# Kernel tuning notes

Measured on AMD Instinct MI355X. Metric: run time of the kernel, lower is better.

## Reference

```python
import jax, jax.numpy as jnp
import numpy as np

EMBED = 512
HEADS = 8
HEAD_DIM = EMBED // HEADS
N, T = 512, 64


def setup_inputs() -> dict:
    key = jax.random.key(0)
    ks = jax.random.split(key, 11)
    s = 1.0 / np.sqrt(EMBED)
    inp = {
        'values': jax.random.normal(ks[0], (N, T, EMBED), jnp.float32),
        'keys':   jax.random.normal(ks[1], (N, T, EMBED), jnp.float32),
        'query':  jax.random.normal(ks[2], (N, T, EMBED), jnp.float32),
        'Wv': jax.random.uniform(ks[3], (EMBED, EMBED), jnp.float32, -s, s),
        'bv': jax.random.uniform(ks[4], (EMBED,), jnp.float32, -s, s),
        'Wk': jax.random.uniform(ks[5], (EMBED, EMBED), jnp.float32, -s, s),
        'bk': jax.random.uniform(ks[6], (EMBED,), jnp.float32, -s, s),
        'Wq': jax.random.uniform(ks[7], (EMBED, EMBED), jnp.float32, -s, s),
        'bq': jax.random.uniform(ks[8], (EMBED,), jnp.float32, -s, s),
        'Wo': jax.random.uniform(ks[9], (EMBED, EMBED), jnp.float32, -s, s),
        'bo': jax.random.uniform(ks[10], (EMBED,), jnp.float32, -s, s),
    }
    return inp


def reference(values, keys, query, Wv, bv, Wk, bk, Wq, bq, Wo, bo):
    n, t, c = query.shape
    v = (values @ Wv.T + bv).reshape(n, t, HEADS, HEAD_DIM)
    k = (keys   @ Wk.T + bk).reshape(n, t, HEADS, HEAD_DIM)
    q = (query  @ Wq.T + bq).reshape(n, t, HEADS, HEAD_DIM)
    # attention over the batch axis: energy[q,k,t,h]
    energy = jnp.einsum('qthd,kthd->qkth', q, k)
    attn = jax.nn.softmax(energy / jnp.sqrt(jnp.float32(EMBED)), axis=1)
    out = jnp.einsum('qkth,kthd->qthd', attn, v).reshape(n, t, HEADS * HEAD_DIM)
    return out @ Wo.T + bo
```

## Files before the change

kernel.cpp:

```cpp
#include <hip/hip_runtime.h>
#include <hip/hip_bf16.h>
#include <math.h>

#define NBATCH 512
#define TT 64
#define EMB 512
#define NHEADS 8
#define HDIM 64
#define MROWS (NBATCH * TT)
#define ROWSTRIDE (TT * EMB)
#define WSEG 262144

static constexpr float QSCALE = 0.0637587140f;

typedef __attribute__((ext_vector_type(8))) short short8v;
typedef __attribute__((ext_vector_type(4))) float f32x4;

__device__ __forceinline__ unsigned short f2bf(float x) {
    union { float f; unsigned int u; } v; v.f = x;
    unsigned int r = v.u + 0x7fff + ((v.u >> 16) & 1);
    return (unsigned short)(r >> 16);
}

__device__ __forceinline__ unsigned int cvtpk(float lo, float hi) {
    unsigned int r;
    asm("v_cvt_pk_bf16_f32 %0, %1, %2" : "=v"(r) : "v"(lo), "v"(hi));
    return r;
}

__device__ __forceinline__ void gl16(const void* g, void* l) {
    __builtin_amdgcn_global_load_lds(
        (const __attribute__((address_space(1))) unsigned int*)g,
        (__attribute__((address_space(3))) unsigned int*)l, 16, 0, 0);
}

__global__ __launch_bounds__(256) void cvt3(
    const float* __restrict__ a, const float* __restrict__ b, const float* __restrict__ c,
    unsigned short* __restrict__ oa, unsigned short* __restrict__ ob, unsigned short* __restrict__ oc)
{
    const size_t i = (size_t)blockIdx.x * 256 + threadIdx.x;
    float4 va = reinterpret_cast<const float4*>(a)[i];
    float4 vb = reinterpret_cast<const float4*>(b)[i];
    float4 vc = reinterpret_cast<const float4*>(c)[i];
    ushort4 ra, rb, rc;
    ra.x = f2bf(va.x); ra.y = f2bf(va.y); ra.z = f2bf(va.z); ra.w = f2bf(va.w);
    rb.x = f2bf(vb.x); rb.y = f2bf(vb.y); rb.z = f2bf(vb.z); rb.w = f2bf(vb.w);
    rc.x = f2bf(vc.x); rc.y = f2bf(vc.y); rc.z = f2bf(vc.z); rc.w = f2bf(vc.w);
    reinterpret_cast<ushort4*>(oa)[i] = ra;
    reinterpret_cast<ushort4*>(ob)[i] = rb;
    reinterpret_cast<ushort4*>(oc)[i] = rc;
}

__global__ __launch_bounds__(256) void cvtw(
    const float* __restrict__ w0, const float* __restrict__ w1,
    const float* __restrict__ w2, const float* __restrict__ w3,
    unsigned short* __restrict__ dst)
{
    const int seg = blockIdx.y;
    const float* src = (seg == 0) ? w0 : (seg == 1) ? w1 : (seg == 2) ? w2 : w3;
    const float sc = (seg == 0) ? QSCALE : 1.0f;
    const size_t i = (size_t)blockIdx.x * 256 + threadIdx.x;
    float4 v = reinterpret_cast<const float4*>(src)[i];
    ushort4 r;
    r.x = f2bf(v.x * sc); r.y = f2bf(v.y * sc); r.z = f2bf(v.z * sc); r.w = f2bf(v.w * sc);
    reinterpret_cast<ushort4*>(dst + (size_t)seg * WSEG)[i] = r;
}

__global__ __launch_bounds__(256) void gemm_proj3(
    const unsigned short* __restrict__ A0, const unsigned short* __restrict__ A1,
    const unsigned short* __restrict__ A2, const unsigned short* __restrict__ Wb,
    const float* __restrict__ b0, const float* __restrict__ b1, const float* __restrict__ b2,
    unsigned short* __restrict__ o0, unsigned short* __restrict__ o1, unsigned short* __restrict__ o2)
{
    __shared__ __align__(16) unsigned short As[128 * 32];
    __shared__ __align__(16) unsigned short Bs[128 * 32];
    const int z = blockIdx.z;
    const unsigned short* A = (z == 0) ? A0 : (z == 1) ? A1 : A2;
    const unsigned short* W = Wb + (size_t)z * WSEG;
    const float* bias = (z == 0) ? b0 : (z == 1) ? b1 : b2;
    const float bsc = (z == 0) ? QSCALE : 1.0f;
    unsigned short* Cout = (z == 0) ? o0 : (z == 1) ? o1 : o2;

    const int tid = threadIdx.x;
    const int wave = tid >> 6, lane = tid & 63;
    const int lg = lane >> 4, li = lane & 15;
    const int m0 = blockIdx.x * 128;
    const int n0 = blockIdx.y * 128;
    const int wr = (wave >> 1) * 64;
    const int wc = (wave & 1) * 64;

    f32x4 acc[4][4] = {};

    const unsigned short* ga = A + (size_t)(m0 + (tid >> 2)) * 512 + (tid & 3) * 8;
    const unsigned short* gb = W + (size_t)(n0 + (tid >> 2)) * 512 + (tid & 3) * 8;
    unsigned short* lA = &As[wave * 512];
    unsigned short* lB = &Bs[wave * 512];

    for (int k0 = 0; k0 < 512; k0 += 32) {
        __syncthreads();
        gl16(ga + k0, lA);
        gl16(ga + k0 + 64 * 512, lA + 2048);
        gl16(gb + k0, lB);
        gl16(gb + k0 + 64 * 512, lB + 2048);
        __syncthreads();

        short8v af[4], bfr[4];
#pragma unroll
        for (int i = 0; i < 4; i++) {
            af[i]  = *reinterpret_cast<const short8v*>(&As[(wr + i * 16 + li) * 32 + lg * 8]);
            bfr[i] = *reinterpret_cast<const short8v*>(&Bs[(wc + i * 16 + li) * 32 + lg * 8]);
        }
#pragma unroll
        for (int i = 0; i < 4; i++)
#pragma unroll
            for (int j = 0; j < 4; j++)
                acc[i][j] = __builtin_amdgcn_mfma_f32_16x16x32_bf16(af[i], bfr[j], acc[i][j], 0, 0, 0);
    }

#pragma unroll
    for (int j = 0; j < 4; j++) {
        const int col = n0 + wc + j * 16 + li;
        const float bb = bias[col] * bsc;
#pragma unroll
        for (int i = 0; i < 4; i++) {
            const int row0 = m0 + wr + i * 16 + lg * 4;
#pragma unroll
            for (int r = 0; r < 4; r++)
                Cout[(size_t)(row0 + r) * 512 + col] = f2bf(acc[i][j][r] + bb);
        }
    }
}

__global__ __launch_bounds__(256) void gemm_out(
    const unsigned short* __restrict__ A, const unsigned short* __restrict__ W,
    const float* __restrict__ bias, float* __restrict__ Cout)
{
    __shared__ __align__(16) unsigned short As[128 * 32];
    __shared__ __align__(16) unsigned short Bs[128 * 32];
    const int tid = threadIdx.x;
    const int wave = tid >> 6, lane = tid & 63;
    const int lg = lane >> 4, li = lane & 15;
    const int m0 = blockIdx.x * 128;
    const int n0 = blockIdx.y * 128;
    const int wr = (wave >> 1) * 64;
    const int wc = (wave & 1) * 64;

    f32x4 acc[4][4] = {};

    const unsigned short* ga = A + (size_t)(m0 + (tid >> 2)) * 512 + (tid & 3) * 8;
    const unsigned short* gb = W + (size_t)(n0 + (tid >> 2)) * 512 + (tid & 3) * 8;
    unsigned short* lA = &As[wave * 512];
    unsigned short* lB = &Bs[wave * 512];

    for (int k0 = 0; k0 < 512; k0 += 32) {
        __syncthreads();
        gl16(ga + k0, lA);
        gl16(ga + k0 + 64 * 512, lA + 2048);
        gl16(gb + k0, lB);
        gl16(gb + k0 + 64 * 512, lB + 2048);
        __syncthreads();

        short8v af[4], bfr[4];
#pragma unroll
        for (int i = 0; i < 4; i++) {
            af[i]  = *reinterpret_cast<const short8v*>(&As[(wr + i * 16 + li) * 32 + lg * 8]);
            bfr[i] = *reinterpret_cast<const short8v*>(&Bs[(wc + i * 16 + li) * 32 + lg * 8]);
        }
#pragma unroll
        for (int i = 0; i < 4; i++)
#pragma unroll
            for (int j = 0; j < 4; j++)
                acc[i][j] = __builtin_amdgcn_mfma_f32_16x16x32_bf16(af[i], bfr[j], acc[i][j], 0, 0, 0);
    }

#pragma unroll
    for (int j = 0; j < 4; j++) {
        const int col = n0 + wc + j * 16 + li;
        const float bb = bias[col];
#pragma unroll
        for (int i = 0; i < 4; i++) {
            const int row0 = m0 + wr + i * 16 + lg * 4;
#pragma unroll
            for (int r = 0; r < 4; r++)
                Cout[(size_t)(row0 + r) * 512 + col] = acc[i][j][r] + bb;
        }
    }
}

__global__ __launch_bounds__(256) void attn_bf16(
    const unsigned short* __restrict__ qp, const unsigned short* __restrict__ kp,
    const unsigned short* __restrict__ vp, unsigned short* __restrict__ ao)
{
    __shared__ __align__(16) unsigned short Qs[128 * 64];
    __shared__ __align__(16) unsigned short Ks[64 * 64];
    __shared__ __align__(16) unsigned short Vt[64][68];
    __shared__ __align__(16) unsigned short Pl[4][32][72];

    const int tid = threadIdx.x;
    const int wave = tid >> 6, lane = tid & 63;
    const int lg = lane >> 4, li = lane & 15;
    const int n0 = blockIdx.x * 128;
    const int th = blockIdx.y;
    const size_t base = (size_t)(th >> 3) * EMB + (size_t)(th & 7) * HDIM;

    {
        const unsigned short* gq = qp + (size_t)(n0 + (tid >> 3)) * ROWSTRIDE + base + (tid & 7) * 8;
        unsigned short* lq = &Qs[wave * 512];
#pragma unroll
        for (int i = 0; i < 4; i++)
            gl16(gq + (size_t)i * 32 * ROWSTRIDE, lq + i * 2048);
    }
    __syncthreads();
    short8v qf[2][2];
#pragma unroll
    for (int mf = 0; mf < 2; mf++)
#pragma unroll
        for (int kf = 0; kf < 2; kf++)
            qf[mf][kf] = *reinterpret_cast<const short8v*>(
                &Qs[(wave * 32 + mf * 16 + li) * 64 + kf * 32 + lg * 8]);

    const int vd0 = (tid & 15) * 4;
    const int vk0 = (tid >> 4) * 4;
    const unsigned short* gv = vp + base + vd0;
    uint2 vl[4];
#pragma unroll
    for (int i = 0; i < 4; i++)
        vl[i] = *reinterpret_cast<const uint2*>(gv + (size_t)(vk0 + i) * ROWSTRIDE);

    const short8v ones = (short8v)(short)0x3F80;
    f32x4 acc[2][4] = {};
    f32x4 acc_l[2] = {};

    for (int kv = 0; kv < 8; kv++) {
        const int k0 = kv * 64;
        __syncthreads();

        {
            unsigned short* lk = &Ks[wave * 512];
#pragma unroll
            for (int i = 0; i < 2; i++) {
                const int r = (tid >> 3) + i * 32;
                const int srcofs = (((tid & 7) * 8) ^ ((r & 7) * 8));
                gl16(kp + (size_t)(k0 + r) * ROWSTRIDE + base + srcofs, lk + i * 2048);
            }
        }
#pragma unroll
        for (int dd = 0; dd < 4; dd++) {
            const unsigned int sel = (dd & 1) ? 0x07060302u : 0x05040100u;
            const unsigned int a = (dd < 2) ? vl[0].x : vl[0].y;
            const unsigned int b = (dd < 2) ? vl[1].x : vl[1].y;
            const unsigned int c = (dd < 2) ? vl[2].x : vl[2].y;
            const unsigned int d = (dd < 2) ? vl[3].x : vl[3].y;
            uint2 o;
            o.x = __builtin_amdgcn_perm(b, a, sel);
            o.y = __builtin_amdgcn_perm(d, c, sel);
            *reinterpret_cast<uint2*>(&Vt[vd0 + dd][vk0]) = o;
        }
        __syncthreads();

        if (kv < 7) {
#pragma unroll
            for (int i = 0; i < 4; i++)
                vl[i] = *reinterpret_cast<const uint2*>(
                    gv + (size_t)(k0 + 64 + vk0 + i) * ROWSTRIDE);
        }

        f32x4 s[2][4] = {};
#pragma unroll
        for (int nf = 0; nf < 4; nf++) {
            const int key = nf * 16 + li;
#pragma unroll
            for (int kf = 0; kf < 2; kf++) {
                const short8v kfrag = *reinterpret_cast<const short8v*>(
                    &Ks[key * 64 + ((kf * 32 + lg * 8) ^ ((key & 7) * 8))]);
#pragma unroll
                for (int mf = 0; mf < 2; mf++)
                    s[mf][nf] = __builtin_amdgcn_mfma_f32_16x16x32_bf16(kfrag, qf[mf][kf], s[mf][nf], 0, 0, 0);
            }
        }

#pragma unroll
        for (int mf = 0; mf < 2; mf++)
#pragma unroll
            for (int nf = 0; nf < 4; nf++) {
                const float p0 = exp2f(s[mf][nf][0]);
                const float p1 = exp2f(s[mf][nf][1]);
                const float p2 = exp2f(s[mf][nf][2]);
                const float p3 = exp2f(s[mf][nf][3]);
                union { unsigned int u[2]; uint2 v; } pk2;
                pk2.u[0] = cvtpk(p0, p1);
                pk2.u[1] = cvtpk(p2, p3);
                *reinterpret_cast<uint2*>(&Pl[wave][mf * 16 + li][nf * 16 + lg * 4]) = pk2.v;
            }

        short8v pf[2][2];
#pragma unroll
        for (int mf = 0; mf < 2; mf++)
#pragma unroll
            for (int kf = 0; kf < 2; kf++)
                pf[mf][kf] = *reinterpret_cast<const short8v*>(
                    &Pl[wave][mf * 16 + li][kf * 32 + lg * 8]);
#pragma unroll
        for (int mf = 0; mf < 2; mf++)
#pragma unroll
            for (int kf = 0; kf < 2; kf++)
                acc_l[mf] = __builtin_amdgcn_mfma_f32_16x16x32_bf16(pf[mf][kf], ones, acc_l[mf], 0, 0, 0);

#pragma unroll
        for (int df = 0; df < 4; df++)
#pragma unroll
            for (int kf = 0; kf < 2; kf++) {
                const short8v vfr = *reinterpret_cast<const short8v*>(
                    &Vt[df * 16 + li][kf * 32 + lg * 8]);
#pragma unroll
                for (int mf = 0; mf < 2; mf++)
                    acc[mf][df] = __builtin_amdgcn_mfma_f32_16x16x32_bf16(pf[mf][kf], vfr, acc[mf][df], 0, 0, 0);
            }
    }

#pragma unroll
    for (int mf = 0; mf < 2; mf++) {
#pragma unroll
        for (int r = 0; r < 4; r++) {
            const float linv = 1.0f / acc_l[mf][r];
            const int qrow = n0 + wave * 32 + mf * 16 + lg * 4 + r;
#pragma unroll
            for (int df = 0; df < 4; df++)
                ao[(size_t)qrow * ROWSTRIDE + base + df * 16 + li] = f2bf(acc[mf][df][r] * linv);
        }
    }
}

extern "C" void kernel_launch(void* const* d_in, const int* in_sizes, int n_in,
                              void* d_out, int out_size, void* d_ws, size_t ws_size,
                              hipStream_t stream) {
    const float* values = (const float*)d_in[0];
    const float* keys   = (const float*)d_in[1];
    const float* query  = (const float*)d_in[2];
    const float* Wv = (const float*)d_in[3];
    const float* bv = (const float*)d_in[4];
    const float* Wk = (const float*)d_in[5];
    const float* bk = (const float*)d_in[6];
    const float* Wq = (const float*)d_in[7];
    const float* bq = (const float*)d_in[8];
    const float* Wo = (const float*)d_in[9];
    const float* bo = (const float*)d_in[10];
    float* out = (float*)d_out;

    unsigned short* ws16 = (unsigned short*)d_ws;
    const size_t PLANE = (size_t)MROWS * EMB;
    unsigned short* xq = ws16;
    unsigned short* xk = ws16 + PLANE;
    unsigned short* xv = ws16 + 2 * PLANE;
    unsigned short* qb = ws16 + 3 * PLANE;
    unsigned short* kb = ws16 + 4 * PLANE;
    unsigned short* vb = ws16 + 5 * PLANE;
    unsigned short* ab = ws16 + 6 * PLANE;
    unsigned short* wb = ws16 + 7 * PLANE;

    cvt3<<<PLANE / 4 / 256, 256, 0, stream>>>(query, keys, values, xq, xk, xv);
    cvtw<<<dim3(WSEG / 4 / 256, 4), 256, 0, stream>>>(Wq, Wk, Wv, Wo, wb);

    gemm_proj3<<<dim3(MROWS / 128, EMB / 128, 3), 256, 0, stream>>>(
        xq, xk, xv, wb, bq, bk, bv, qb, kb, vb);

    attn_bf16<<<dim3(4, TT * NHEADS), 256, 0, stream>>>(qb, kb, vb, ab);

    gemm_out<<<dim3(MROWS / 128, EMB / 128), 256, 0, stream>>>(
        ab, wb + 3 * WSEG, bo, out);
}
```

Before: 245.7 us.

## Fuse fp32-to-bf16 activation conversion into projection GEMM A-tile load

Removes the separate cvt3 kernel, which read three fp32 activation planes and wrote bf16 copies. The projection GEMM now loads fp32 A tiles straight into LDS with an XOR-swizzled layout and converts them to bf16 with v_cvt_pk_bf16_f32 when building MFMA fragments. This drops one kernel launch and a full bf16 write plus re-read of the activations. In exchange each of the four column blocks reloads fp32 A (twice the bytes), LDS use doubles and conversion work moves inside the GEMM inner loop.

```diff
diff --git a/kernel.cpp b/kernel.cpp
--- a/kernel.cpp
+++ b/kernel.cpp
@@ -32,23 +32,6 @@
     __builtin_amdgcn_global_load_lds(
         (const __attribute__((address_space(1))) unsigned int*)g,
         (__attribute__((address_space(3))) unsigned int*)l, 16, 0, 0);
-}
-
-__global__ __launch_bounds__(256) void cvt3(
-    const float* __restrict__ a, const float* __restrict__ b, const float* __restrict__ c,
-    unsigned short* __restrict__ oa, unsigned short* __restrict__ ob, unsigned short* __restrict__ oc)
-{
-    const size_t i = (size_t)blockIdx.x * 256 + threadIdx.x;
-    float4 va = reinterpret_cast<const float4*>(a)[i];
-    float4 vb = reinterpret_cast<const float4*>(b)[i];
-    float4 vc = reinterpret_cast<const float4*>(c)[i];
-    ushort4 ra, rb, rc;
-    ra.x = f2bf(va.x); ra.y = f2bf(va.y); ra.z = f2bf(va.z); ra.w = f2bf(va.w);
-    rb.x = f2bf(vb.x); rb.y = f2bf(vb.y); rb.z = f2bf(vb.z); rb.w = f2bf(vb.w);
-    rc.x = f2bf(vc.x); rc.y = f2bf(vc.y); rc.z = f2bf(vc.z); rc.w = f2bf(vc.w);
-    reinterpret_cast<ushort4*>(oa)[i] = ra;
-    reinterpret_cast<ushort4*>(ob)[i] = rb;
-    reinterpret_cast<ushort4*>(oc)[i] = rc;
 }
 
 __global__ __launch_bounds__(256) void cvtw(
@@ -67,15 +50,15 @@
 }
 
 __global__ __launch_bounds__(256) void gemm_proj3(
-    const unsigned short* __restrict__ A0, const unsigned short* __restrict__ A1,
-    const unsigned short* __restrict__ A2, const unsigned short* __restrict__ Wb,
+    const float* __restrict__ A0, const float* __restrict__ A1,
+    const float* __restrict__ A2, const unsigned short* __restrict__ Wb,
     const float* __restrict__ b0, const float* __restrict__ b1, const float* __restrict__ b2,
     unsigned short* __restrict__ o0, unsigned short* __restrict__ o1, unsigned short* __restrict__ o2)
 {
-    __shared__ __align__(16) unsigned short As[128 * 32];
+    __shared__ __align__(16) float Asf[128 * 32];
     __shared__ __align__(16) unsigned short Bs[128 * 32];
     const int z = blockIdx.z;
-    const unsigned short* A = (z == 0) ? A0 : (z == 1) ? A1 : A2;
+    const float* A = (z == 0) ? A0 : (z == 1) ? A1 : A2;
     const unsigned short* W = Wb + (size_t)z * WSEG;
     const float* bias = (z == 0) ? b0 : (z == 1) ? b1 : b2;
     const float bsc = (z == 0) ? QSCALE : 1.0f;
@@ -91,15 +74,18 @@
 
     f32x4 acc[4][4] = {};
 
-    const unsigned short* ga = A + (size_t)(m0 + (tid >> 2)) * 512 + (tid & 3) * 8;
+    const int asrc_unit = (tid & 7) ^ ((tid >> 3) & 7);
+    const float* gaf = A + (size_t)(m0 + (tid >> 3)) * 512 + asrc_unit * 4;
+    float* lA = Asf + wave * 256;
     const unsigned short* gb = W + (size_t)(n0 + (tid >> 2)) * 512 + (tid & 3) * 8;
-    unsigned short* lA = &As[wave * 512];
     unsigned short* lB = &Bs[wave * 512];
 
     for (int k0 = 0; k0 < 512; k0 += 32) {
         __syncthreads();
-        gl16(ga + k0, lA);
-        gl16(ga + k0 + 64 * 512, lA + 2048);
+        gl16(gaf + k0, lA);
+        gl16(gaf + k0 + 32 * 512, lA + 1024);
+        gl16(gaf + k0 + 64 * 512, lA + 2048);
+        gl16(gaf + k0 + 96 * 512, lA + 3072);
         gl16(gb + k0, lB);
         gl16(gb + k0 + 64 * 512, lB + 2048);
         __syncthreads();
@@ -107,7 +93,16 @@
         short8v af[4], bfr[4];
 #pragma unroll
         for (int i = 0; i < 4; i++) {
-            af[i]  = *reinterpret_cast<const short8v*>(&As[(wr + i * 16 + li) * 32 + lg * 8]);
+            const int r = wr + i * 16 + li;
+            const int rx = r & 7;
+            const float4 fa = *reinterpret_cast<const float4*>(
+                &Asf[r * 32 + ((lg * 2) ^ rx) * 4]);
+            const float4 fb = *reinterpret_cast<const float4*>(
+                &Asf[r * 32 + ((lg * 2 + 1) ^ rx) * 4]);
+            union { unsigned int u[4]; short8v v; } pk;
+            pk.u[0] = cvtpk(fa.x, fa.y); pk.u[1] = cvtpk(fa.z, fa.w);
+            pk.u[2] = cvtpk(fb.x, fb.y); pk.u[3] = cvtpk(fb.z, fb.w);
+            af[i] = pk.v;
             bfr[i] = *reinterpret_cast<const short8v*>(&Bs[(wc + i * 16 + li) * 32 + lg * 8]);
         }
 #pragma unroll
@@ -349,20 +344,16 @@
 
     unsigned short* ws16 = (unsigned short*)d_ws;
     const size_t PLANE = (size_t)MROWS * EMB;
-    unsigned short* xq = ws16;
-    unsigned short* xk = ws16 + PLANE;
-    unsigned short* xv = ws16 + 2 * PLANE;
-    unsigned short* qb = ws16 + 3 * PLANE;
-    unsigned short* kb = ws16 + 4 * PLANE;
-    unsigned short* vb = ws16 + 5 * PLANE;
-    unsigned short* ab = ws16 + 6 * PLANE;
-    unsigned short* wb = ws16 + 7 * PLANE;
-
-    cvt3<<<PLANE / 4 / 256, 256, 0, stream>>>(query, keys, values, xq, xk, xv);
+    unsigned short* qb = ws16;
+    unsigned short* kb = ws16 + PLANE;
+    unsigned short* vb = ws16 + 2 * PLANE;
+    unsigned short* ab = ws16 + 3 * PLANE;
+    unsigned short* wb = ws16 + 4 * PLANE;
+
     cvtw<<<dim3(WSEG / 4 / 256, 4), 256, 0, stream>>>(Wq, Wk, Wv, Wo, wb);
 
     gemm_proj3<<<dim3(MROWS / 128, EMB / 128, 3), 256, 0, stream>>>(
-        xq, xk, xv, wb, bq, bk, bv, qb, kb, vb);
+        query, keys, values, wb, bq, bk, bv, qb, kb, vb);
 
     attn_bf16<<<dim3(4, TT * NHEADS), 256, 0, stream>>>(qb, kb, vb, ab);
 
```

After: 245.0 us. No clear change (-0.3%).
